# Performance work log

Hardware: AMD Instinct MI355X
Metric: run time of the kernel (lower is better)

## Reference

```python
import jax, jax.numpy as jnp
import numpy as np

N_NODES = 100000
N_EDGES = 1600000
IN_FT = 128
OUT_FT = 128


def gcn_conv(x, W, b, src, dst, n):
    """PyG-style GCNConv: add self-loops, symmetric normalization, linear."""
    h = x @ W  # [n, out]
    loop = jnp.arange(n, dtype=src.dtype)
    s = jnp.concatenate([src, loop])  # sources (x_j)
    d = jnp.concatenate([dst, loop])  # targets (aggregation index)
    deg = jax.ops.segment_sum(jnp.ones(s.shape[0], dtype=h.dtype), d, num_segments=n)
    dinv = jnp.where(deg > 0, jax.lax.rsqrt(deg), 0.0)
    norm = dinv[s] * dinv[d]  # [E+n]
    msg = h[s] * norm[:, None]  # gather + scale
    out = jax.ops.segment_sum(msg, d, num_segments=n)  # scatter-add
    return out + b


def setup_inputs() -> dict:
    key = jax.random.key(0)
    ks = jax.random.split(key, 12)
    def lin(kw, kb, fan_in, fan_out):
        bound = 1.0 / np.sqrt(fan_in)
        W = jax.random.uniform(kw, (fan_in, fan_out), jnp.float32, -bound, bound)
        b = jax.random.uniform(kb, (fan_out,), jnp.float32, -bound, bound)
        return W, b
    x = jax.random.normal(ks[0], (N_NODES, IN_FT), jnp.float32)
    edge_index = jax.random.randint(ks[1], (2, N_EDGES), 0, N_NODES, jnp.int64)
    proj_W, proj_b = lin(ks[2], ks[3], IN_FT, OUT_FT)
    W1, b1 = lin(ks[4], ks[5], IN_FT, OUT_FT)
    W2, b2 = lin(ks[6], ks[7], 2 * OUT_FT, OUT_FT)
    W3, b3 = lin(ks[8], ks[9], 3 * OUT_FT, OUT_FT)
    return {"x": x, "edge_index": edge_index, "proj_W": proj_W, "proj_b": proj_b,
            "W1": W1, "b1": b1, "W2": W2, "b2": b2, "W3": W3, "b3": b3}


def reference(x, edge_index, proj_W, proj_b, W1, b1, W2, b2, W3, b3):
    n = x.shape[0]
    src, dst = edge_index[0], edge_index[1]
    act = jax.nn.relu
    x_p = act(x @ proj_W + proj_b)
    h1 = act(gcn_conv(x, W1, b1, src, dst, n))
    in2 = jnp.concatenate([x_p, h1], axis=1)
    h2 = act(gcn_conv(in2, W2, b2, src, dst, n))
    in3 = jnp.concatenate([x_p, h1, h2], axis=1)
    h3 = act(gcn_conv(in3, W3, b3, src, dst, n))
    return h3
```

## Files before the change

kernel.cpp:

```cpp
#include <hip/hip_runtime.h>

#define N_NODES 100000
#define N_EDGES 1600000

typedef __attribute__((ext_vector_type(8))) short bf16x8;
typedef __attribute__((ext_vector_type(4))) float f32x4;
typedef __attribute__((ext_vector_type(2))) float f32x2;
typedef __attribute__((ext_vector_type(4))) unsigned short u16x4;

__device__ __forceinline__ float b2f(unsigned short u) {
    union { unsigned int i; float f; } v; v.i = ((unsigned int)u) << 16; return v.f;
}
__device__ __forceinline__ unsigned short f2b(float f) {
    union { float ff; unsigned int i; } v; v.ff = f;
    unsigned int x = v.i;
    x += 0x7fffu + ((x >> 16) & 1u);
    return (unsigned short)(x >> 16);
}

__global__ __launch_bounds__(256) void k_cast4(const float* __restrict__ in,
                                               unsigned short* __restrict__ out, int n4) {
    int i = blockIdx.x * 256 + threadIdx.x;
    if (i < n4) {
        f32x4 v = *(const f32x4*)&in[(size_t)i * 4];
        u16x4 o;
        o[0] = f2b(v[0]); o[1] = f2b(v[1]); o[2] = f2b(v[2]); o[3] = f2b(v[3]);
        *(u16x4*)&out[(size_t)i * 4] = o;
    }
}

__global__ __launch_bounds__(256) void k_castWT(
    const float* __restrict__ pW, const float* __restrict__ W1,
    const float* __restrict__ W2, const float* __restrict__ W3,
    unsigned short* __restrict__ out)
{
    int i = blockIdx.x * 256 + threadIdx.x;
    if (i >= 114688) return;
    const float* src; int K, base;
    if (i < 16384)      { src = pW; K = 128; base = 0; }
    else if (i < 32768) { src = W1; K = 128; base = 16384; }
    else if (i < 65536) { src = W2; K = 256; base = 32768; }
    else                { src = W3; K = 384; base = 65536; }
    int loc = i - base;
    int col = loc / K, k = loc - col * K;
    out[i] = f2b(src[(size_t)k * 128 + col]);
}

#define SCAT_GROUPS 8
#define SCAT_WIN ((N_NODES + SCAT_GROUPS - 1) / SCAT_GROUPS)
#define BUCKET_CAP 204800
#define PART_BLOCKS 782
#define PART_EPB 2048
#define HIST_BLOCKS 2048
#define SCAT_BLOCKS 2048

__global__ void k_init_deg(int* deg, int* gcur) {
    int i = blockIdx.x * 256 + threadIdx.x;
    if (i < N_NODES) deg[i] = 1;
    if (i < SCAT_GROUPS) gcur[i] = i * BUCKET_CAP;
}

__global__ __launch_bounds__(256) void k_part(
    const int* __restrict__ src, const int* __restrict__ dst,
    int* __restrict__ gcur, unsigned long long* __restrict__ part)
{
    __shared__ int bcnt[8];
    __shared__ int lcur[8];
    const int tid = threadIdx.x;
    const int ll  = tid & 63;
    const int base = blockIdx.x * PART_EPB;
    int sv[8], dv[8], bv[8];
    int mycnt[8] = {0, 0, 0, 0, 0, 0, 0, 0};
#pragma unroll
    for (int u = 0; u < 8; ++u) {
        int e = base + u * 256 + tid;
        bool val = e < N_EDGES;
        sv[u] = val ? src[e] : 0;
        dv[u] = val ? dst[e] : 0;
        bv[u] = val ? dv[u] / SCAT_WIN : -1;
#pragma unroll
        for (int bk = 0; bk < 8; ++bk) mycnt[bk] += (bv[u] == bk);
    }
    if (tid < 8) bcnt[tid] = 0;
    __syncthreads();
#pragma unroll
    for (int bk = 0; bk < 8; ++bk) {
        int c = mycnt[bk];
        for (int o = 1; o < 64; o <<= 1) c += __shfl_xor(c, o, 64);
        if (ll == 0 && c) atomicAdd(&bcnt[bk], c);
    }
    __syncthreads();
    if (tid < 8) lcur[tid] = atomicAdd(&gcur[tid], bcnt[tid]);
    __syncthreads();
#pragma unroll
    for (int u = 0; u < 8; ++u) {
        unsigned long long masks[8]; int cnts[8];
#pragma unroll
        for (int bk = 0; bk < 8; ++bk) {
            masks[bk] = __ballot(bv[u] == bk);
            cnts[bk]  = __popcll(masks[bk]);
        }
        int posv = 0;
        if (ll < 8) posv = atomicAdd(&lcur[ll], cnts[ll]);
        int myoff = 0;
#pragma unroll
        for (int bk = 0; bk < 8; ++bk) {
            int bb = __builtin_amdgcn_readlane(posv, bk);
            if (bv[u] == bk) myoff = bb + __popcll(masks[bk] & ((1ULL << ll) - 1ULL));
        }
        if (bv[u] >= 0)
            part[myoff] = ((unsigned long long)(unsigned)dv[u] << 32) | (unsigned)sv[u];
    }
}

__global__ __launch_bounds__(256) void k_hist2(
    const unsigned long long* __restrict__ part, const int* __restrict__ gcur,
    int* __restrict__ deg)
{
    const int w  = blockIdx.x & (SCAT_GROUPS - 1);
    const int g  = blockIdx.x >> 3;
    const int b0 = w * BUCKET_CAP;
    const int cnt = gcur[w] - b0;
    const int stride = (HIST_BLOCKS / SCAT_GROUPS) * 256;
    for (int i = g * 256 + threadIdx.x; i < cnt; i += stride) {
        int d = (int)(part[b0 + i] >> 32);
        atomicAdd(&deg[d], 1);
    }
}

#define SCAN_CHUNK 2048
#define SCAN_BLOCKS ((N_NODES + SCAN_CHUNK - 1) / SCAN_CHUNK)

__global__ __launch_bounds__(256) void k_deg_part(const int* __restrict__ deg,
                                                  int* __restrict__ psum) {
    int b = blockIdx.x, t = threadIdx.x;
    int base = b * SCAN_CHUNK + t * 8;
    int s = 0;
#pragma unroll
    for (int i = 0; i < 8; ++i) { int idx = base + i; if (idx < N_NODES) s += deg[idx]; }
    for (int o = 1; o < 64; o <<= 1) s += __shfl_xor(s, o, 64);
    __shared__ int ws[4];
    if ((t & 63) == 0) ws[t >> 6] = s;
    __syncthreads();
    if (t == 0) psum[b] = ws[0] + ws[1] + ws[2] + ws[3];
}

__global__ void k_scan_off(const int* __restrict__ psum, int* __restrict__ poff) {
    int t = threadIdx.x;
    int v = (t < SCAN_BLOCKS) ? psum[t] : 0;
    int sc = v;
    for (int o = 1; o < 64; o <<= 1) { int u = __shfl_up(sc, o, 64); if (t >= o) sc += u; }
    if (t < SCAN_BLOCKS) poff[t] = sc - v;
}

__global__ __launch_bounds__(256) void k_scan_final(
    const int* __restrict__ deg, const int* __restrict__ poff,
    int* __restrict__ row_ptr, int* __restrict__ cursor, float* __restrict__ dinv)
{
    int b = blockIdx.x, t = threadIdx.x;
    int base = b * SCAN_CHUNK + t * 8;
    int v[8]; int s = 0;
#pragma unroll
    for (int i = 0; i < 8; ++i) { int idx = base + i; v[i] = (idx < N_NODES) ? deg[idx] : 0; s += v[i]; }
    int lane = t & 63, wv = t >> 6;
    int sc = s;
    for (int o = 1; o < 64; o <<= 1) { int u = __shfl_up(sc, o, 64); if (lane >= o) sc += u; }
    __shared__ int wsum[4];
    if (lane == 63) wsum[wv] = sc;
    __syncthreads();
    int woff = 0;
    for (int i = 0; i < wv; ++i) woff += wsum[i];
    int excl = poff[b] + woff + sc - s;
#pragma unroll
    for (int i = 0; i < 8; ++i) {
        int idx = base + i;
        if (idx < N_NODES) {
            row_ptr[idx] = excl; cursor[idx] = excl;
            dinv[idx] = rsqrtf((float)v[i]);
            excl += v[i];
        }
    }
}

__global__ __launch_bounds__(256) void k_scat2(
    const unsigned long long* __restrict__ part, const int* __restrict__ gcur,
    int* __restrict__ cursor, int* __restrict__ ssrc)
{
    const int w  = blockIdx.x & (SCAT_GROUPS - 1);
    const int g  = blockIdx.x >> 3;
    const int b0 = w * BUCKET_CAP;
    const int cnt = gcur[w] - b0;
    const int stride = (SCAT_BLOCKS / SCAT_GROUPS) * 256;
    for (int i = g * 256 + threadIdx.x; i < cnt; i += stride) {
        unsigned long long e = part[b0 + i];
        int d = (int)(e >> 32);
        int s = (int)(e & 0xffffffffu);
        int p = atomicAdd(&cursor[d], 1);
        ssrc[p] = s;
    }
}

template<int NC, bool RELU, bool BIAS, bool SCALE>
__global__ __launch_bounds__(256) void k_gemm(
    const unsigned short* __restrict__ A0, const unsigned short* __restrict__ A1,
    const unsigned short* __restrict__ A2, const unsigned short* __restrict__ WtG,
    const float* __restrict__ bias, const float* __restrict__ dinv,
    unsigned short* __restrict__ out)
{
    const int tid  = threadIdx.x;
    const int wave = tid >> 6, lane = tid & 63;
    const int l15 = lane & 15, lg = lane >> 4;
    const int K = NC * 128;
    const int rbase = blockIdx.x * 128 + wave * 32;

    f32x4 acc[2][8];
#pragma unroll
    for (int i = 0; i < 2; ++i)
#pragma unroll
        for (int j = 0; j < 8; ++j) acc[i][j] = (f32x4)(0.0f);

    int ar0 = rbase + l15;      if (ar0 >= N_NODES) ar0 = N_NODES - 1;
    int ar1 = rbase + 16 + l15; if (ar1 >= N_NODES) ar1 = N_NODES - 1;

    for (int c = 0; c < NC; ++c) {
        const unsigned short* Ac = (c == 0) ? A0 : ((c == 1) ? A1 : A2);
#pragma unroll
        for (int ks = 0; ks < 4; ++ks) {
            const int ko = ks * 32 + lg * 8;
            bf16x8 a0 = *(const bf16x8*)&Ac[(size_t)ar0 * 128 + ko];
            bf16x8 a1 = *(const bf16x8*)&Ac[(size_t)ar1 * 128 + ko];
#pragma unroll
            for (int cf = 0; cf < 8; ++cf) {
                bf16x8 b = *(const bf16x8*)&WtG[(size_t)(cf * 16 + l15) * K + c * 128 + ko];
                acc[0][cf] = __builtin_amdgcn_mfma_f32_16x16x32_bf16(a0, b, acc[0][cf], 0, 0, 0);
                acc[1][cf] = __builtin_amdgcn_mfma_f32_16x16x32_bf16(a1, b, acc[1][cf], 0, 0, 0);
            }
        }
    }
    float bvs[8];
#pragma unroll
    for (int cf = 0; cf < 8; ++cf) bvs[cf] = BIAS ? bias[cf * 16 + l15] : 0.0f;
#pragma unroll
    for (int ai = 0; ai < 2; ++ai) {
#pragma unroll
        for (int j = 0; j < 4; ++j) {
            int row = rbase + ai * 16 + lg * 4 + j;
            if (row < N_NODES) {
                float sc = SCALE ? dinv[row] : 1.0f;
#pragma unroll
                for (int cf = 0; cf < 8; ++cf) {
                    float v = acc[ai][cf][j] + bvs[cf];
                    if (RELU)  v = fmaxf(v, 0.0f);
                    if (SCALE) v *= sc;
                    out[(size_t)row * 128 + cf * 16 + l15] = f2b(v);
                }
            }
        }
    }
}

template<bool FINAL>
__global__ __launch_bounds__(256) void k_agg(
    const unsigned short* __restrict__ t, const int* __restrict__ ssrc,
    const int* __restrict__ row_ptr, const int* __restrict__ deg,
    const float* __restrict__ dinv, const float* __restrict__ bias,
    void* __restrict__ out_v)
{
    const int wave = threadIdx.x >> 6;
    const int lane = threadIdx.x & 63;
    const int node = blockIdx.x * 4 + wave;
    if (node >= N_NODES) return;

    const int beg = row_ptr[node];
    const int cnt = deg[node] - 1;
    float a0 = 0.0f, a1 = 0.0f;

    for (int kb = 0; kb < cnt; kb += 64) {
        const int rem = cnt - kb;
        const int lim = rem < 64 ? rem : 64;
        int sk = 0;
        if (lane < lim) sk = ssrc[beg + kb + lane];

        int k = 0;
        for (; k + 8 <= lim; k += 8) {
            unsigned int p[8];
#pragma unroll
            for (int u = 0; u < 8; ++u) {
                int s = __builtin_amdgcn_readlane(sk, k + u);
                p[u] = *(const unsigned int*)&t[(size_t)s * 128 + lane * 2];
            }
#pragma unroll
            for (int u = 0; u < 8; ++u) {
                a0 += b2f((unsigned short)(p[u] & 0xffffu));
                a1 += b2f((unsigned short)(p[u] >> 16));
            }
        }
        for (; k < lim; ++k) {
            int s0 = __builtin_amdgcn_readlane(sk, k);
            unsigned int p0 = *(const unsigned int*)&t[(size_t)s0 * 128 + lane * 2];
            a0 += b2f((unsigned short)(p0 & 0xffffu));
            a1 += b2f((unsigned short)(p0 >> 16));
        }
    }

    unsigned int ps = *(const unsigned int*)&t[(size_t)node * 128 + lane * 2];
    a0 += b2f((unsigned short)(ps & 0xffffu));
    a1 += b2f((unsigned short)(ps >> 16));

    float di = dinv[node];
    f32x2 bv = *(const f32x2*)&bias[lane * 2];
    float o0 = fmaxf(di * a0 + bv[0], 0.0f);
    float o1 = fmaxf(di * a1 + bv[1], 0.0f);
    if (FINAL) {
        f32x2 po; po[0] = o0; po[1] = o1;
        *(f32x2*)((float*)out_v + (size_t)node * 128 + lane * 2) = po;
    } else {
        unsigned short* out = (unsigned short*)out_v;
        unsigned int po = (unsigned int)f2b(o0) | ((unsigned int)f2b(o1) << 16);
        *(unsigned int*)&out[(size_t)node * 128 + lane * 2] = po;
    }
}

extern "C" void kernel_launch(void* const* d_in, const int* in_sizes, int n_in,
                              void* d_out, int out_size, void* d_ws, size_t ws_size,
                              hipStream_t stream)
{
    const float* x  = (const float*)d_in[0];
    const int*   ei = (const int*)d_in[1];
    const float* pW = (const float*)d_in[2];
    const float* pb = (const float*)d_in[3];
    const float* W1 = (const float*)d_in[4];
    const float* b1 = (const float*)d_in[5];
    const float* W2 = (const float*)d_in[6];
    const float* b2 = (const float*)d_in[7];
    const float* W3 = (const float*)d_in[8];
    const float* b3 = (const float*)d_in[9];
    const int* src = ei;
    const int* dst = ei + N_EDGES;

    char* ws = (char*)d_ws;
    size_t off = 0;
    auto alloc = [&](size_t bytes) -> char* {
        char* p = ws + off; off += (bytes + 255) & ~(size_t)255; return p;
    };
    const size_t NB = (size_t)N_NODES * 128;
    unsigned short* xb = (unsigned short*)alloc(NB * 2);
    unsigned short* xp = (unsigned short*)alloc(NB * 2);
    unsigned short* h1 = (unsigned short*)alloc(NB * 2);
    unsigned short* h2 = (unsigned short*)alloc(NB * 2);
    unsigned short* tb = (unsigned short*)alloc(NB * 2);
    unsigned short* Wb = (unsigned short*)alloc((size_t)114688 * 2);
    int*   deg  = (int*)alloc((size_t)N_NODES * 4);
    int*   rp   = (int*)alloc((size_t)N_NODES * 4);
    int*   cur  = (int*)alloc((size_t)N_NODES * 4);
    float* dinv = (float*)alloc((size_t)N_NODES * 4);
    int*   psum = (int*)alloc((size_t)SCAN_BLOCKS * 4);
    int*   poff = (int*)alloc((size_t)SCAN_BLOCKS * 4);
    int*   gcur = (int*)alloc((size_t)SCAT_GROUPS * 4);
    int*   ssrc = (int*)alloc((size_t)(N_EDGES + N_NODES) * 4);

    unsigned long long* part = (unsigned long long*)tb;

    unsigned short* pWt = Wb;
    unsigned short* W1t = Wb + 16384;
    unsigned short* W2t = Wb + 32768;
    unsigned short* W3t = Wb + 65536;

    k_cast4<<<(int)(NB / 4 + 255) / 256, 256, 0, stream>>>(x, xb, (int)(NB / 4));
    k_castWT<<<(114688 + 255) / 256, 256, 0, stream>>>(pW, W1, W2, W3, Wb);

    k_init_deg<<<(N_NODES + 255) / 256, 256, 0, stream>>>(deg, gcur);
    k_part<<<PART_BLOCKS, 256, 0, stream>>>(src, dst, gcur, part);
    k_hist2<<<HIST_BLOCKS, 256, 0, stream>>>(part, gcur, deg);
    k_deg_part<<<SCAN_BLOCKS, 256, 0, stream>>>(deg, psum);
    k_scan_off<<<1, 64, 0, stream>>>(psum, poff);
    k_scan_final<<<SCAN_BLOCKS, 256, 0, stream>>>(deg, poff, rp, cur, dinv);
    k_scat2<<<SCAT_BLOCKS, 256, 0, stream>>>(part, gcur, cur, ssrc);

    const int gblocks = (N_NODES + 127) / 128;
    const int ablocks = (N_NODES + 3) / 4;

    k_gemm<1, true,  true,  false><<<gblocks, 256, 0, stream>>>(xb, nullptr, nullptr, pWt, pb, dinv, xp);
    k_gemm<1, false, false, true ><<<gblocks, 256, 0, stream>>>(xb, nullptr, nullptr, W1t, nullptr, dinv, tb);
    k_agg<false><<<ablocks, 256, 0, stream>>>(tb, ssrc, rp, deg, dinv, b1, h1);
    k_gemm<2, false, false, true ><<<gblocks, 256, 0, stream>>>(xp, h1, nullptr, W2t, nullptr, dinv, tb);
    k_agg<false><<<ablocks, 256, 0, stream>>>(tb, ssrc, rp, deg, dinv, b2, h2);
    k_gemm<3, false, false, true ><<<gblocks, 256, 0, stream>>>(xp, h1, h2, W3t, nullptr, dinv, tb);
    k_agg<true><<<ablocks, 256, 0, stream>>>(tb, ssrc, rp, deg, dinv, b3, d_out);
}
```

Measured before the change: 649.2 us.

## Add second-level edge partition so degree count and CSR fill use LDS atomics

Edges are split a second time into 256 fine windows of about 391 destination nodes each. Degree histogramming and the CSR scatter then run one block per window, using shared-memory counters and cursors instead of global atomics on 100k-entry arrays. This removes the global deg init and the cursor array, at the cost of an extra partition pass over 1.6M 8-byte edges. It also relies on each fine bucket holding at most 8192 edges (CAP2), which is safe for uniform random graphs but would overflow on skewed ones.

```diff
diff --git a/kernel.cpp b/kernel.cpp
--- a/kernel.cpp
+++ b/kernel.cpp
@@ -46,65 +46,68 @@
     out[i] = f2b(src[(size_t)k * 128 + col]);
 }
 
-#define SCAT_GROUPS 8
-#define SCAT_WIN ((N_NODES + SCAT_GROUPS - 1) / SCAT_GROUPS)
-#define BUCKET_CAP 204800
+#define NB1 8
+#define WIN1 ((N_NODES + NB1 - 1) / NB1)
+#define CAP1 204800
 #define PART_BLOCKS 782
 #define PART_EPB 2048
-#define HIST_BLOCKS 2048
-#define SCAT_BLOCKS 2048
-
-__global__ void k_init_deg(int* deg, int* gcur) {
-    int i = blockIdx.x * 256 + threadIdx.x;
-    if (i < N_NODES) deg[i] = 1;
-    if (i < SCAT_GROUPS) gcur[i] = i * BUCKET_CAP;
+#define SUBS 32
+#define NWIN (NB1 * SUBS)
+#define WIN2 ((WIN1 + SUBS - 1) / SUBS)
+#define CAP2 8192
+#define PART2_BLOCKS 2048
+
+__global__ void k_init(int* gcur, int* gcur2) {
+    int i = threadIdx.x;
+    if (i < NB1)  gcur[i]  = i * CAP1;
+    if (i < NWIN) gcur2[i] = i * CAP2;
 }
 
 __global__ __launch_bounds__(256) void k_part(
     const int* __restrict__ src, const int* __restrict__ dst,
     int* __restrict__ gcur, unsigned long long* __restrict__ part)
 {
-    __shared__ int bcnt[8];
-    __shared__ int lcur[8];
+    __shared__ int bcnt[NB1];
+    __shared__ int lcur[NB1];
     const int tid = threadIdx.x;
     const int ll  = tid & 63;
     const int base = blockIdx.x * PART_EPB;
     int sv[8], dv[8], bv[8];
-    int mycnt[8] = {0, 0, 0, 0, 0, 0, 0, 0};
+    int mycnt[NB1] = {0, 0, 0, 0, 0, 0, 0, 0};
 #pragma unroll
     for (int u = 0; u < 8; ++u) {
         int e = base + u * 256 + tid;
         bool val = e < N_EDGES;
         sv[u] = val ? src[e] : 0;
         dv[u] = val ? dst[e] : 0;
-        bv[u] = val ? dv[u] / SCAT_WIN : -1;
-#pragma unroll
-        for (int bk = 0; bk < 8; ++bk) mycnt[bk] += (bv[u] == bk);
-    }
-    if (tid < 8) bcnt[tid] = 0;
-    __syncthreads();
-#pragma unroll
-    for (int bk = 0; bk < 8; ++bk) {
+        bv[u] = val ? dv[u] / WIN1 : -1;
+#pragma unroll
+        for (int bk = 0; bk < NB1; ++bk) mycnt[bk] += (bv[u] == bk);
+    }
+    if (tid < NB1) bcnt[tid] = 0;
+    __syncthreads();
+#pragma unroll
+    for (int bk = 0; bk < NB1; ++bk) {
         int c = mycnt[bk];
         for (int o = 1; o < 64; o <<= 1) c += __shfl_xor(c, o, 64);
         if (ll == 0 && c) atomicAdd(&bcnt[bk], c);
     }
     __syncthreads();
-    if (tid < 8) lcur[tid] = atomicAdd(&gcur[tid], bcnt[tid]);
+    if (tid < NB1) lcur[tid] = atomicAdd(&gcur[tid], bcnt[tid]);
     __syncthreads();
 #pragma unroll
     for (int u = 0; u < 8; ++u) {
-        unsigned long long masks[8]; int cnts[8];
-#pragma unroll
-        for (int bk = 0; bk < 8; ++bk) {
+        unsigned long long masks[NB1]; int cnts[NB1];
+#pragma unroll
+        for (int bk = 0; bk < NB1; ++bk) {
             masks[bk] = __ballot(bv[u] == bk);
             cnts[bk]  = __popcll(masks[bk]);
         }
         int posv = 0;
-        if (ll < 8) posv = atomicAdd(&lcur[ll], cnts[ll]);
+        if (ll < NB1) posv = atomicAdd(&lcur[ll], cnts[ll]);
         int myoff = 0;
 #pragma unroll
-        for (int bk = 0; bk < 8; ++bk) {
+        for (int bk = 0; bk < NB1; ++bk) {
             int bb = __builtin_amdgcn_readlane(posv, bk);
             if (bv[u] == bk) myoff = bb + __popcll(masks[bk] & ((1ULL << ll) - 1ULL));
         }
@@ -113,19 +116,67 @@
     }
 }
 
-__global__ __launch_bounds__(256) void k_hist2(
+__global__ __launch_bounds__(256) void k_part2(
     const unsigned long long* __restrict__ part, const int* __restrict__ gcur,
+    int* __restrict__ gcur2, unsigned long long* __restrict__ part2)
+{
+    __shared__ int bcnt[SUBS];
+    __shared__ int lcur[SUBS];
+    const int w   = blockIdx.x & (NB1 - 1);
+    const int g   = blockIdx.x >> 3;
+    const int tid = threadIdx.x;
+    const int b0  = w * CAP1;
+    const int cnt = gcur[w] - b0;
+    const int chunk = (cnt + 255) >> 8;
+    const int lo = g * chunk;
+    const int hi = min(lo + chunk, cnt);
+    const int rounds = (hi > lo) ? ((hi - lo + 255) >> 8) : 0;
+    const int nlo_base = w * WIN1;
+
+    unsigned long long ev[4];
+    int bkv[4];
+    if (tid < SUBS) bcnt[tid] = 0;
+    __syncthreads();
+    for (int r = 0; r < rounds; ++r) {
+        int i = lo + r * 256 + tid;
+        bool val = i < hi;
+        unsigned long long e = val ? part[b0 + i] : 0ULL;
+        int bk = val ? ((int)(e >> 32) - nlo_base) / WIN2 : -1;
+        ev[r] = e; bkv[r] = bk;
+        if (val) atomicAdd(&bcnt[bk], 1);
+    }
+    __syncthreads();
+    if (tid < SUBS) lcur[tid] = atomicAdd(&gcur2[w * SUBS + tid], bcnt[tid]);
+    __syncthreads();
+    for (int r = 0; r < rounds; ++r) {
+        int mybk = bkv[r];
+        if (mybk >= 0) {
+            int off = atomicAdd(&lcur[mybk], 1);
+            part2[off] = ev[r];
+        }
+    }
+}
+
+__global__ __launch_bounds__(512) void k_histw(
+    const unsigned long long* __restrict__ part2, const int* __restrict__ gcur2,
     int* __restrict__ deg)
 {
-    const int w  = blockIdx.x & (SCAT_GROUPS - 1);
-    const int g  = blockIdx.x >> 3;
-    const int b0 = w * BUCKET_CAP;
-    const int cnt = gcur[w] - b0;
-    const int stride = (HIST_BLOCKS / SCAT_GROUPS) * 256;
-    for (int i = g * 256 + threadIdx.x; i < cnt; i += stride) {
-        int d = (int)(part[b0 + i] >> 32);
-        atomicAdd(&deg[d], 1);
-    }
+    __shared__ int cnt[WIN2];
+    const int q = blockIdx.x;
+    const int w = q >> 5, s = q & (SUBS - 1);
+    const int nlo = w * WIN1 + s * WIN2;
+    const int nhi = w * WIN1 + min((s + 1) * WIN2, WIN1);
+    const int wn = nhi - nlo;
+    for (int i = threadIdx.x; i < wn; i += 512) cnt[i] = 0;
+    __syncthreads();
+    const int b0 = q * CAP2;
+    const int ec = gcur2[q] - b0;
+    for (int i = threadIdx.x; i < ec; i += 512) {
+        int d = (int)(part2[b0 + i] >> 32);
+        atomicAdd(&cnt[d - nlo], 1);
+    }
+    __syncthreads();
+    for (int i = threadIdx.x; i < wn; i += 512) deg[nlo + i] = cnt[i] + 1;
 }
 
 #define SCAN_CHUNK 2048
@@ -155,7 +206,7 @@
 
 __global__ __launch_bounds__(256) void k_scan_final(
     const int* __restrict__ deg, const int* __restrict__ poff,
-    int* __restrict__ row_ptr, int* __restrict__ cursor, float* __restrict__ dinv)
+    int* __restrict__ row_ptr, float* __restrict__ dinv)
 {
     int b = blockIdx.x, t = threadIdx.x;
     int base = b * SCAN_CHUNK + t * 8;
@@ -175,28 +226,32 @@
     for (int i = 0; i < 8; ++i) {
         int idx = base + i;
         if (idx < N_NODES) {
-            row_ptr[idx] = excl; cursor[idx] = excl;
+            row_ptr[idx] = excl;
             dinv[idx] = rsqrtf((float)v[i]);
             excl += v[i];
         }
     }
 }
 
-__global__ __launch_bounds__(256) void k_scat2(
-    const unsigned long long* __restrict__ part, const int* __restrict__ gcur,
-    int* __restrict__ cursor, int* __restrict__ ssrc)
-{
-    const int w  = blockIdx.x & (SCAT_GROUPS - 1);
-    const int g  = blockIdx.x >> 3;
-    const int b0 = w * BUCKET_CAP;
-    const int cnt = gcur[w] - b0;
-    const int stride = (SCAT_BLOCKS / SCAT_GROUPS) * 256;
-    for (int i = g * 256 + threadIdx.x; i < cnt; i += stride) {
-        unsigned long long e = part[b0 + i];
+__global__ __launch_bounds__(512) void k_sortw(
+    const unsigned long long* __restrict__ part2, const int* __restrict__ gcur2,
+    const int* __restrict__ row_ptr, int* __restrict__ ssrc)
+{
+    __shared__ int cur[WIN2];
+    const int q = blockIdx.x;
+    const int w = q >> 5, s = q & (SUBS - 1);
+    const int nlo = w * WIN1 + s * WIN2;
+    const int nhi = w * WIN1 + min((s + 1) * WIN2, WIN1);
+    const int wn = nhi - nlo;
+    for (int i = threadIdx.x; i < wn; i += 512) cur[i] = row_ptr[nlo + i];
+    __syncthreads();
+    const int b0 = q * CAP2;
+    const int ec = gcur2[q] - b0;
+    for (int i = threadIdx.x; i < ec; i += 512) {
+        unsigned long long e = part2[b0 + i];
         int d = (int)(e >> 32);
-        int s = (int)(e & 0xffffffffu);
-        int p = atomicAdd(&cursor[d], 1);
-        ssrc[p] = s;
+        int p = atomicAdd(&cur[d - nlo], 1);
+        ssrc[p] = (int)(e & 0xffffffffu);
     }
 }
 
@@ -352,14 +407,15 @@
     unsigned short* Wb = (unsigned short*)alloc((size_t)114688 * 2);
     int*   deg  = (int*)alloc((size_t)N_NODES * 4);
     int*   rp   = (int*)alloc((size_t)N_NODES * 4);
-    int*   cur  = (int*)alloc((size_t)N_NODES * 4);
     float* dinv = (float*)alloc((size_t)N_NODES * 4);
     int*   psum = (int*)alloc((size_t)SCAN_BLOCKS * 4);
     int*   poff = (int*)alloc((size_t)SCAN_BLOCKS * 4);
-    int*   gcur = (int*)alloc((size_t)SCAT_GROUPS * 4);
+    int*   gcur = (int*)alloc((size_t)NB1 * 4);
+    int*   gcur2= (int*)alloc((size_t)NWIN * 4);
     int*   ssrc = (int*)alloc((size_t)(N_EDGES + N_NODES) * 4);
 
-    unsigned long long* part = (unsigned long long*)tb;
+    unsigned long long* part  = (unsigned long long*)tb;
+    unsigned long long* part2 = (unsigned long long*)h2;
 
     unsigned short* pWt = Wb;
     unsigned short* W1t = Wb + 16384;
@@ -369,13 +425,14 @@
     k_cast4<<<(int)(NB / 4 + 255) / 256, 256, 0, stream>>>(x, xb, (int)(NB / 4));
     k_castWT<<<(114688 + 255) / 256, 256, 0, stream>>>(pW, W1, W2, W3, Wb);
 
-    k_init_deg<<<(N_NODES + 255) / 256, 256, 0, stream>>>(deg, gcur);
+    k_init<<<1, 512, 0, stream>>>(gcur, gcur2);
     k_part<<<PART_BLOCKS, 256, 0, stream>>>(src, dst, gcur, part);
-    k_hist2<<<HIST_BLOCKS, 256, 0, stream>>>(part, gcur, deg);
+    k_part2<<<PART2_BLOCKS, 256, 0, stream>>>(part, gcur, gcur2, part2);
+    k_histw<<<NWIN, 512, 0, stream>>>(part2, gcur2, deg);
     k_deg_part<<<SCAN_BLOCKS, 256, 0, stream>>>(deg, psum);
     k_scan_off<<<1, 64, 0, stream>>>(psum, poff);
-    k_scan_final<<<SCAN_BLOCKS, 256, 0, stream>>>(deg, poff, rp, cur, dinv);
-    k_scat2<<<SCAT_BLOCKS, 256, 0, stream>>>(part, gcur, cur, ssrc);
+    k_scan_final<<<SCAN_BLOCKS, 256, 0, stream>>>(deg, poff, rp, dinv);
+    k_sortw<<<NWIN, 512, 0, stream>>>(part2, gcur2, rp, ssrc);
 
     const int gblocks = (N_NODES + 127) / 128;
     const int ablocks = (N_NODES + 3) / 4;
```

Measured after the change: 548.3 us. 15.5% less time.
